# Kernel tuning notes

Measured on AMD Instinct MI355X. Metric: run time of the kernel, lower is better.

Reference implementation:

```python
import jax, jax.numpy as jnp
import numpy as np

N = 10000
E = 320000
C = 16


def gcn_conv(x, edge_index, W, b, num_nodes):
    # PyG GCNConv: h = X W, then symmetric-normalized aggregation with self-loops, then + b
    h = x @ W  # [N, F_out]
    loop = jnp.arange(num_nodes, dtype=edge_index.dtype)
    src = jnp.concatenate([edge_index[0], loop])
    dst = jnp.concatenate([edge_index[1], loop])
    ones = jnp.ones(src.shape[0], dtype=h.dtype)
    deg = jax.ops.segment_sum(ones, dst, num_segments=num_nodes)  # in-degree incl. self-loop
    dinv = jnp.where(deg > 0, jax.lax.rsqrt(deg), 0.0)
    norm = dinv[src] * dinv[dst]  # [E+N]
    msg = h[src] * norm[:, None]  # gather + scale
    out = jax.ops.segment_sum(msg, dst, num_segments=num_nodes)  # scatter-add
    return out + b


def setup_inputs() -> dict:
    key = jax.random.key(0)
    ks = jax.random.split(key, 8)
    x = jax.random.normal(ks[0], (N, N), dtype=jnp.float32)
    edge_index = jax.random.randint(ks[1], (2, E), 0, N, dtype=jnp.int64)
    W1 = jax.random.normal(ks[2], (N, 64), dtype=jnp.float32) * (1.0 / np.sqrt(N))
    b1 = jnp.zeros((64,), dtype=jnp.float32)
    W2 = jax.random.normal(ks[3], (64, 64), dtype=jnp.float32) * (1.0 / 8.0)
    b2 = jnp.zeros((64,), dtype=jnp.float32)
    W3 = jax.random.normal(ks[4], (64, C), dtype=jnp.float32) * (1.0 / 8.0)
    b3 = jnp.zeros((C,), dtype=jnp.float32)
    return {"x": x, "edge_index": edge_index, "W1": W1, "b1": b1,
            "W2": W2, "b2": b2, "W3": W3, "b3": b3}


def reference(x, edge_index, W1, b1, W2, b2, W3, b3):
    h = jax.nn.relu(gcn_conv(x, edge_index, W1, b1, N))
    h = jax.nn.relu(gcn_conv(h, edge_index, W2, b2, N))
    h = gcn_conv(h, edge_index, W3, b3, N)
    return jax.nn.softmax(h, axis=1)
```

## Files before the change

kernel.cpp:

```cpp
#include <hip/hip_runtime.h>

#define N_NODES 10000
#define E_EDGES 320000
#define KP 10016

typedef float f32x4 __attribute__((ext_vector_type(4)));
typedef __bf16 bf16x8 __attribute__((ext_vector_type(8)));

static __device__ __forceinline__ ushort f2bf(float f) {
    unsigned u = __float_as_uint(f);
    unsigned r = (u + 0x7fffu + ((u >> 16) & 1u)) >> 16;
    return (ushort)r;
}
static __device__ __forceinline__ float bf2f(ushort h) {
    return __uint_as_float(((unsigned)h) << 16);
}


__global__ void k_hist(const int* __restrict__ dst, int* __restrict__ deg) {
    int e = blockIdx.x * blockDim.x + threadIdx.x;
    if (e < E_EDGES) atomicAdd(&deg[dst[e]], 1);
}

__global__ void k_dinv(const int* __restrict__ deg, float* __restrict__ dinv) {
    int i = blockIdx.x * blockDim.x + threadIdx.x;
    if (i < N_NODES) dinv[i] = rsqrtf(1.0f + (float)deg[i]);
}

__global__ void k_scan(const int* __restrict__ deg, int* __restrict__ roff) {
    __shared__ int sums[256];
    __shared__ int offs[256];
    const int CH = 40;
    int t = threadIdx.x;
    int base = t * CH;
    int s = 0;
    for (int i = 0; i < CH; i++) {
        int idx = base + i;
        if (idx < N_NODES) s += deg[idx];
    }
    sums[t] = s;
    __syncthreads();
    if (t == 0) {
        int r = 0;
        for (int i = 0; i < 256; i++) { offs[i] = r; r += sums[i]; }
    }
    __syncthreads();
    int r = offs[t];
    for (int i = 0; i < CH; i++) {
        int idx = base + i;
        if (idx < N_NODES) { roff[idx] = r; r += deg[idx]; }
    }
    if (t == 255) roff[N_NODES] = E_EDGES;
}

__global__ void k_scatter(const int* __restrict__ src, const int* __restrict__ dst,
                          const int* __restrict__ roff, int* __restrict__ cursor,
                          const float* __restrict__ dinv,
                          int* __restrict__ csrc, float* __restrict__ cw) {
    int e = blockIdx.x * blockDim.x + threadIdx.x;
    if (e >= E_EDGES) return;
    int s = src[e], d = dst[e];
    int slot = roff[d] + atomicAdd(&cursor[d], 1);
    csrc[slot] = s;
    cw[slot] = dinv[s] * dinv[d];
}


__global__ void k_wsplit(const float* __restrict__ W1, ushort* __restrict__ Whi,
                         ushort* __restrict__ Wlo) {
    int k = blockIdx.x * 256 + threadIdx.x;
    int n = blockIdx.y;
    if (k >= KP) return;
    ushort h = 0, l = 0;
    if (k < N_NODES) {
        float f = W1[(long)k * 64 + n];
        h = f2bf(f);
        l = f2bf(f - bf2f(h));
    }
    Whi[(long)n * KP + k] = h;
    Wlo[(long)n * KP + k] = l;
}


#define G1_BM 128
#define G1_CHUNK 1280

__global__ __launch_bounds__(256) void k_gemm1_mfma(
        const float* __restrict__ x, const ushort* __restrict__ Whi,
        const ushort* __restrict__ Wlo, float* __restrict__ out) {
    __shared__ ushort As[2][G1_BM][40];
    __shared__ ushort Bs[2][64][40];

    int tid = threadIdx.x;
    int lane = tid & 63, wv = tid >> 6;
    int quad = lane >> 4, lm = lane & 15;
    int q8 = quad * 8;
    int m0 = blockIdx.x * G1_BM;
    int ks = blockIdx.y * G1_CHUNK;
    int ke = min(ks + G1_CHUNK, N_NODES);

    f32x4 acc[2][4] = {};

    int bn = tid >> 2, bp = (tid & 3) * 8;

    for (int k0 = ks; k0 < ke; k0 += 32) {
#pragma unroll
        for (int i = 0; i < 4; i++) {
            int f = tid + i * 256;
            int row = f >> 3, kq = f & 7;
            int gm = m0 + row, gk = k0 + kq * 4;
            float4 v = make_float4(0.f, 0.f, 0.f, 0.f);
            if (gm < N_NODES && gk < N_NODES)
                v = *(const float4*)(x + (long)gm * N_NODES + gk);
            ushort h0 = f2bf(v.x), h1 = f2bf(v.y), h2 = f2bf(v.z), h3 = f2bf(v.w);
            ushort l0 = f2bf(v.x - bf2f(h0)), l1 = f2bf(v.y - bf2f(h1));
            ushort l2 = f2bf(v.z - bf2f(h2)), l3 = f2bf(v.w - bf2f(h3));
            *(ushort4*)&As[0][row][kq * 4] = make_ushort4(h0, h1, h2, h3);
            *(ushort4*)&As[1][row][kq * 4] = make_ushort4(l0, l1, l2, l3);
        }
        *(float4*)&Bs[0][bn][bp] = *(const float4*)&Whi[(long)bn * KP + k0 + bp];
        *(float4*)&Bs[1][bn][bp] = *(const float4*)&Wlo[(long)bn * KP + k0 + bp];
        __syncthreads();

        bf16x8 ah[2], al[2], bh[4], bl[4];
#pragma unroll
        for (int r = 0; r < 2; r++) {
            int row = wv * 32 + r * 16 + lm;
            ah[r] = *(const bf16x8*)&As[0][row][q8];
            al[r] = *(const bf16x8*)&As[1][row][q8];
        }
#pragma unroll
        for (int c = 0; c < 4; c++) {
            int n = c * 16 + lm;
            bh[c] = *(const bf16x8*)&Bs[0][n][q8];
            bl[c] = *(const bf16x8*)&Bs[1][n][q8];
        }
#pragma unroll
        for (int r = 0; r < 2; r++)
#pragma unroll
            for (int c = 0; c < 4; c++) {
                acc[r][c] = __builtin_amdgcn_mfma_f32_16x16x32_bf16(al[r], bh[c], acc[r][c], 0, 0, 0);
                acc[r][c] = __builtin_amdgcn_mfma_f32_16x16x32_bf16(ah[r], bl[c], acc[r][c], 0, 0, 0);
                acc[r][c] = __builtin_amdgcn_mfma_f32_16x16x32_bf16(ah[r], bh[c], acc[r][c], 0, 0, 0);
            }
        __syncthreads();
    }

#pragma unroll
    for (int r = 0; r < 2; r++)
#pragma unroll
        for (int c = 0; c < 4; c++) {
            int row0 = m0 + wv * 32 + r * 16 + quad * 4;
            int cn = c * 16 + lm;
#pragma unroll
            for (int i = 0; i < 4; i++) {
                int gm = row0 + i;
                if (gm < N_NODES) atomicAdd(&out[gm * 64 + cn], acc[r][c][i]);
            }
        }
}


__global__ void k_gemm64(const float* __restrict__ in, const float* __restrict__ W,
                         float* __restrict__ out) {
    __shared__ float Ws[64 * 64];
    __shared__ float Ain[4][64];
    int tid = threadIdx.x;
    int tx = tid & 63, ty = tid >> 6;
    for (int f = tid; f < 1024; f += 256)
        *(float4*)&Ws[f * 4] = *(const float4*)&W[f * 4];
    int gm = blockIdx.x * 4 + ty;
    Ain[ty][tx] = in[gm * 64 + tx];
    __syncthreads();
    float acc = 0.f;
#pragma unroll
    for (int k = 0; k < 64; k++) acc = fmaf(Ain[ty][k], Ws[k * 64 + tx], acc);
    out[gm * 64 + tx] = acc;
}

__global__ void k_gemm16(const float* __restrict__ in, const float* __restrict__ W,
                         float* __restrict__ out) {
    __shared__ float Ws[64 * 16];
    __shared__ float Ain[16][64];
    int tid = threadIdx.x;
    int tx = tid & 15, ty = tid >> 4;
    *(float4*)&Ws[tid * 4] = *(const float4*)&W[tid * 4];
    {
        int r = tid >> 4, kq = tid & 15;
        *(float4*)&Ain[r][kq * 4] =
            *(const float4*)(in + (long)(blockIdx.x * 16 + r) * 64 + kq * 4);
    }
    __syncthreads();
    float acc = 0.f;
#pragma unroll
    for (int k = 0; k < 64; k++) acc = fmaf(Ain[ty][k], Ws[k * 16 + tx], acc);
    out[(blockIdx.x * 16 + ty) * 16 + tx] = acc;
}


__global__ void k_agg64(const float* __restrict__ h, const float* __restrict__ bias,
                        const int* __restrict__ roff, const int* __restrict__ csrc,
                        const float* __restrict__ cw, const float* __restrict__ dinv,
                        float* __restrict__ out, int do_relu) {
    int n = blockIdx.x * 4 + (threadIdx.x >> 6);
    int c = threadIdx.x & 63;
    float di = dinv[n];
    float acc = di * di * h[n * 64 + c];
    int e0 = roff[n], e1 = roff[n + 1];
    int e = e0;
    for (; e + 3 < e1; e += 4) {
        int s0 = csrc[e], s1 = csrc[e + 1], s2 = csrc[e + 2], s3 = csrc[e + 3];
        float w0 = cw[e], w1 = cw[e + 1], w2 = cw[e + 2], w3 = cw[e + 3];
        float v0 = h[s0 * 64 + c], v1 = h[s1 * 64 + c];
        float v2 = h[s2 * 64 + c], v3 = h[s3 * 64 + c];
        acc = fmaf(w0, v0, acc);
        acc = fmaf(w1, v1, acc);
        acc = fmaf(w2, v2, acc);
        acc = fmaf(w3, v3, acc);
    }
    for (; e < e1; e++)
        acc = fmaf(cw[e], h[csrc[e] * 64 + c], acc);
    acc += bias[c];
    if (do_relu) acc = fmaxf(acc, 0.f);
    out[n * 64 + c] = acc;
}

__global__ void k_agg16_softmax(const float* __restrict__ h, const float* __restrict__ b3,
                                const int* __restrict__ roff, const int* __restrict__ csrc,
                                const float* __restrict__ cw, const float* __restrict__ dinv,
                                float* __restrict__ out) {
    int lane = threadIdx.x & 63;
    int n = blockIdx.x * 4 + (threadIdx.x >> 6);
    int c = lane & 15, g = lane >> 4;
    float di = dinv[n];
    float acc = (g == 0) ? di * di * h[n * 16 + c] : 0.f;
    int e0 = roff[n], e1 = roff[n + 1];
    for (int e = e0 + g; e < e1; e += 4)
        acc = fmaf(cw[e], h[csrc[e] * 16 + c], acc);
    acc += __shfl_xor(acc, 16);
    acc += __shfl_xor(acc, 32);
    float logit = acc + b3[c];
    float m = logit;
    m = fmaxf(m, __shfl_xor(m, 1));
    m = fmaxf(m, __shfl_xor(m, 2));
    m = fmaxf(m, __shfl_xor(m, 4));
    m = fmaxf(m, __shfl_xor(m, 8));
    float ex = expf(logit - m);
    float s = ex;
    s += __shfl_xor(s, 1);
    s += __shfl_xor(s, 2);
    s += __shfl_xor(s, 4);
    s += __shfl_xor(s, 8);
    if (g == 0) out[n * 16 + c] = ex / s;
}


extern "C" void kernel_launch(void* const* d_in, const int* in_sizes, int n_in,
                              void* d_out, int out_size, void* d_ws, size_t ws_size,
                              hipStream_t stream) {
    (void)in_sizes; (void)n_in; (void)out_size; (void)ws_size;
    const float* x  = (const float*)d_in[0];
    const int*   ei = (const int*)d_in[1];
    const float* W1 = (const float*)d_in[2];
    const float* b1 = (const float*)d_in[3];
    const float* W2 = (const float*)d_in[4];
    const float* b2 = (const float*)d_in[5];
    const float* W3 = (const float*)d_in[6];
    const float* b3 = (const float*)d_in[7];
    float* out = (float*)d_out;
    const int* esrc = ei;
    const int* edst = ei + E_EDGES;

    char* p = (char*)d_ws;
    size_t off = 0;
    auto alloc = [&](size_t b) -> void* {
        void* r = p + off;
        off += (b + 255) & ~(size_t)255;
        return r;
    };
    int*    deg    = (int*)alloc(N_NODES * 4);
    int*    cursor = (int*)alloc(N_NODES * 4);
    int*    roff   = (int*)alloc((N_NODES + 1) * 4);
    float*  dinv   = (float*)alloc(N_NODES * 4);
    int*    csrc   = (int*)alloc(E_EDGES * 4);
    float*  cw     = (float*)alloc(E_EDGES * 4);
    float*  bufA   = (float*)alloc(N_NODES * 64 * 4);
    float*  bufB   = (float*)alloc(N_NODES * 64 * 4);
    float*  bufC   = (float*)alloc(N_NODES * 16 * 4);
    ushort* Whi    = (ushort*)alloc((size_t)64 * KP * 2);
    ushort* Wlo    = (ushort*)alloc((size_t)64 * KP * 2);

    hipMemsetAsync(deg, 0, N_NODES * 4, stream);
    hipMemsetAsync(cursor, 0, N_NODES * 4, stream);
    hipMemsetAsync(bufA, 0, N_NODES * 64 * 4, stream);

    k_hist<<<(E_EDGES + 255) / 256, 256, 0, stream>>>(edst, deg);
    k_dinv<<<(N_NODES + 255) / 256, 256, 0, stream>>>(deg, dinv);
    k_scan<<<1, 256, 0, stream>>>(deg, roff);
    k_scatter<<<(E_EDGES + 255) / 256, 256, 0, stream>>>(esrc, edst, roff, cursor, dinv,
                                                         csrc, cw);
    k_wsplit<<<dim3((KP + 255) / 256, 64), 256, 0, stream>>>(W1, Whi, Wlo);

    k_gemm1_mfma<<<dim3((N_NODES + G1_BM - 1) / G1_BM, 8), 256, 0, stream>>>(x, Whi, Wlo, bufA);
    k_agg64<<<N_NODES / 4, 256, 0, stream>>>(bufA, b1, roff, csrc, cw, dinv, bufB, 1);
    k_gemm64<<<N_NODES / 4, 256, 0, stream>>>(bufB, W2, bufA);
    k_agg64<<<N_NODES / 4, 256, 0, stream>>>(bufA, b2, roff, csrc, cw, dinv, bufB, 1);
    k_gemm16<<<N_NODES / 16, 256, 0, stream>>>(bufB, W3, bufC);
    k_agg16_softmax<<<N_NODES / 4, 256, 0, stream>>>(bufC, b3, roff, csrc, cw, dinv, out);
}
```

Baseline: 716.8 us.

## Load X tiles directly to LDS and split to bf16 at fragment read

The first GEMM now copies raw fp32 X tiles into a swizzled LDS buffer with global_load_lds, instead of going through registers. The hi/lo bf16 split moves to the fragment read, using a cheaper truncation split based on perm. The K range is cut into 16 chunks of 640 instead of 8 of 1280 to raise parallelism. Out-of-range reads are clamped rather than zeroed, relying on zero padding in W past N. Truncating instead of rounding changes the hi/lo split slightly, and more chunks mean more atomic adds at the output.

Result: faster. 687.9 us (-4.0%).

```diff
diff --git a/kernel.cpp b/kernel.cpp
--- a/kernel.cpp
+++ b/kernel.cpp
@@ -6,6 +6,8 @@
 
 typedef float f32x4 __attribute__((ext_vector_type(4)));
 typedef __bf16 bf16x8 __attribute__((ext_vector_type(8)));
+
+union frag_u { int4 i; bf16x8 b; };
 
 static __device__ __forceinline__ ushort f2bf(float f) {
     unsigned u = __float_as_uint(f);
@@ -14,6 +16,22 @@
 }
 static __device__ __forceinline__ float bf2f(ushort h) {
     return __uint_as_float(((unsigned)h) << 16);
+}
+
+static __device__ __forceinline__ void split2(float f0, float f1,
+                                              unsigned& hi, unsigned& lo) {
+    unsigned u0 = __float_as_uint(f0), u1 = __float_as_uint(f1);
+    hi = __builtin_amdgcn_perm(u1, u0, 0x07060302u);
+    float h0 = __uint_as_float(u0 & 0xFFFF0000u);
+    float h1 = __uint_as_float(u1 & 0xFFFF0000u);
+    float l0 = f0 - h0, l1 = f1 - h1;
+    lo = __builtin_amdgcn_perm(__float_as_uint(l1), __float_as_uint(l0), 0x07060302u);
+}
+
+static __device__ __forceinline__ void load16_to_lds(const float* gp, void* lp) {
+    __builtin_amdgcn_global_load_lds(
+        (__attribute__((address_space(1))) void*)(gp),
+        (__attribute__((address_space(3))) void*)(lp), 16, 0, 0);
 }
 
 
@@ -83,65 +101,83 @@
 
 
 #define G1_BM 128
-#define G1_CHUNK 1280
+#define G1_CHUNK 640
+#define G1_NCHUNK 16
 
 __global__ __launch_bounds__(256) void k_gemm1_mfma(
         const float* __restrict__ x, const ushort* __restrict__ Whi,
         const ushort* __restrict__ Wlo, float* __restrict__ out) {
-    __shared__ ushort As[2][G1_BM][40];
+    __shared__ float As32[G1_BM][32];
     __shared__ ushort Bs[2][64][40];
 
     int tid = threadIdx.x;
     int lane = tid & 63, wv = tid >> 6;
     int quad = lane >> 4, lm = lane & 15;
-    int q8 = quad * 8;
     int m0 = blockIdx.x * G1_BM;
     int ks = blockIdx.y * G1_CHUNK;
-    int ke = min(ks + G1_CHUNK, N_NODES);
+    int ke = min(ks + G1_CHUNK, KP);
+
+    int rown = lane >> 3;
+    int sp = (lane & 7) ^ rown;
+    long abase[4];
+#pragma unroll
+    for (int i = 0; i < 4; i++) {
+        int row = (wv * 4 + i) * 8 + rown;
+        int gm = min(m0 + row, N_NODES - 1);
+        abase[i] = (long)gm * N_NODES + sp * 4;
+    }
+    const long FLAT_MAX = (long)N_NODES * N_NODES - 4;
+
+    int bn = tid >> 2, bp = (tid & 3) * 8;
+    const ushort* whip = Whi + (long)bn * KP + bp;
+    const ushort* wlop = Wlo + (long)bn * KP + bp;
 
     f32x4 acc[2][4] = {};
 
-    int bn = tid >> 2, bp = (tid & 3) * 8;
-
     for (int k0 = ks; k0 < ke; k0 += 32) {
 #pragma unroll
         for (int i = 0; i < 4; i++) {
-            int f = tid + i * 256;
-            int row = f >> 3, kq = f & 7;
-            int gm = m0 + row, gk = k0 + kq * 4;
-            float4 v = make_float4(0.f, 0.f, 0.f, 0.f);
-            if (gm < N_NODES && gk < N_NODES)
-                v = *(const float4*)(x + (long)gm * N_NODES + gk);
-            ushort h0 = f2bf(v.x), h1 = f2bf(v.y), h2 = f2bf(v.z), h3 = f2bf(v.w);
-            ushort l0 = f2bf(v.x - bf2f(h0)), l1 = f2bf(v.y - bf2f(h1));
-            ushort l2 = f2bf(v.z - bf2f(h2)), l3 = f2bf(v.w - bf2f(h3));
-            *(ushort4*)&As[0][row][kq * 4] = make_ushort4(h0, h1, h2, h3);
-            *(ushort4*)&As[1][row][kq * 4] = make_ushort4(l0, l1, l2, l3);
+            long flat = abase[i] + k0;
+            if (flat > FLAT_MAX) flat = FLAT_MAX;
+            load16_to_lds(x + flat, &As32[(wv * 4 + i) * 8][0]);
         }
-        *(float4*)&Bs[0][bn][bp] = *(const float4*)&Whi[(long)bn * KP + k0 + bp];
-        *(float4*)&Bs[1][bn][bp] = *(const float4*)&Wlo[(long)bn * KP + k0 + bp];
+        float4 vh = *(const float4*)(whip + k0);
+        float4 vl = *(const float4*)(wlop + k0);
+        *(float4*)&Bs[0][bn][bp] = vh;
+        *(float4*)&Bs[1][bn][bp] = vl;
         __syncthreads();
 
-        bf16x8 ah[2], al[2], bh[4], bl[4];
+        frag_u ah[2], al[2];
 #pragma unroll
         for (int r = 0; r < 2; r++) {
             int row = wv * 32 + r * 16 + lm;
-            ah[r] = *(const bf16x8*)&As[0][row][q8];
-            al[r] = *(const bf16x8*)&As[1][row][q8];
+            int r7 = row & 7;
+            int s0 = (quad * 2) ^ r7;
+            int s1 = (quad * 2 + 1) ^ r7;
+            float4 fa = *(const float4*)&As32[row][s0 * 4];
+            float4 fb = *(const float4*)&As32[row][s1 * 4];
+            unsigned h0, l0, h1, l1, h2, l2, h3, l3;
+            split2(fa.x, fa.y, h0, l0);
+            split2(fa.z, fa.w, h1, l1);
+            split2(fb.x, fb.y, h2, l2);
+            split2(fb.z, fb.w, h3, l3);
+            ah[r].i = make_int4((int)h0, (int)h1, (int)h2, (int)h3);
+            al[r].i = make_int4((int)l0, (int)l1, (int)l2, (int)l3);
         }
+        frag_u bh[4], bl[4];
 #pragma unroll
         for (int c = 0; c < 4; c++) {
             int n = c * 16 + lm;
-            bh[c] = *(const bf16x8*)&Bs[0][n][q8];
-            bl[c] = *(const bf16x8*)&Bs[1][n][q8];
+            bh[c].b = *(const bf16x8*)&Bs[0][n][quad * 8];
+            bl[c].b = *(const bf16x8*)&Bs[1][n][quad * 8];
         }
 #pragma unroll
         for (int r = 0; r < 2; r++)
 #pragma unroll
             for (int c = 0; c < 4; c++) {
-                acc[r][c] = __builtin_amdgcn_mfma_f32_16x16x32_bf16(al[r], bh[c], acc[r][c], 0, 0, 0);
-                acc[r][c] = __builtin_amdgcn_mfma_f32_16x16x32_bf16(ah[r], bl[c], acc[r][c], 0, 0, 0);
-                acc[r][c] = __builtin_amdgcn_mfma_f32_16x16x32_bf16(ah[r], bh[c], acc[r][c], 0, 0, 0);
+                acc[r][c] = __builtin_amdgcn_mfma_f32_16x16x32_bf16(al[r].b, bh[c].b, acc[r][c], 0, 0, 0);
+                acc[r][c] = __builtin_amdgcn_mfma_f32_16x16x32_bf16(ah[r].b, bl[c].b, acc[r][c], 0, 0, 0);
+                acc[r][c] = __builtin_amdgcn_mfma_f32_16x16x32_bf16(ah[r].b, bh[c].b, acc[r][c], 0, 0, 0);
             }
         __syncthreads();
     }
@@ -301,7 +337,8 @@
                                                          csrc, cw);
     k_wsplit<<<dim3((KP + 255) / 256, 64), 256, 0, stream>>>(W1, Whi, Wlo);
 
-    k_gemm1_mfma<<<dim3((N_NODES + G1_BM - 1) / G1_BM, 8), 256, 0, stream>>>(x, Whi, Wlo, bufA);
+    k_gemm1_mfma<<<dim3((N_NODES + G1_BM - 1) / G1_BM, G1_NCHUNK), 256, 0, stream>>>(
+        x, Whi, Wlo, bufA);
     k_agg64<<<N_NODES / 4, 256, 0, stream>>>(bufA, b1, roff, csrc, cw, dinv, bufB, 1);
     k_gemm64<<<N_NODES / 4, 256, 0, stream>>>(bufB, W2, bufA);
     k_agg64<<<N_NODES / 4, 256, 0, stream>>>(bufA, b2, roff, csrc, cw, dinv, bufB, 1);
```
